# Optimization experiments

Measured on AMD Instinct MI355X. Metric: run time of the kernel, lower is better.

Reference implementation:

```python
import jax, jax.numpy as jnp
import numpy as np

N, B, DIN = 128, 2, 128
D, DFF, NHEAD, NLAYERS = 256, 1024, 8, 2
BLOCK = 32
LENGTH = 160


def setup_inputs() -> dict:
    key = jax.random.key(0)
    ks = jax.random.split(key, 10)
    r = lambda k, sh: jax.random.normal(k, sh, jnp.float32) * 0.05
    return {
        "inputs": jax.random.normal(ks[0], (N, B, DIN), jnp.float32),
        "in_W1": r(ks[1], (DIN, DFF)), "in_b1": jnp.zeros((DFF,), jnp.float32),
        "in_W2": r(ks[2], (DFF, D)), "in_b2": jnp.zeros((D,), jnp.float32),
        "k_W1": r(ks[3], (DIN, DFF)), "k_b1": jnp.zeros((DFF,), jnp.float32),
        "k_W2": r(ks[4], (DFF, 2)), "k_b2": jnp.zeros((2,), jnp.float32),
        "Wqkv": r(ks[5], (NLAYERS, D, 3 * D)), "bqkv": jnp.zeros((NLAYERS, 3 * D), jnp.float32),
        "Wo": r(ks[6], (NLAYERS, D, D)), "bo": jnp.zeros((NLAYERS, D), jnp.float32),
        "ln1_g": jnp.ones((NLAYERS, D), jnp.float32), "ln1_b": jnp.zeros((NLAYERS, D), jnp.float32),
        "W1": r(ks[7], (NLAYERS, D, DFF)), "b1": jnp.zeros((NLAYERS, DFF), jnp.float32),
        "W2": r(ks[8], (NLAYERS, DFF, D)), "b2": jnp.zeros((NLAYERS, D), jnp.float32),
        "ln2_g": jnp.ones((NLAYERS, D), jnp.float32), "ln2_b": jnp.zeros((NLAYERS, D), jnp.float32),
        "length": LENGTH,
    }


def _ln(x, g, b):
    m = jnp.mean(x, axis=-1, keepdims=True)
    v = jnp.mean(jnp.square(x - m), axis=-1, keepdims=True)
    return (x - m) * jax.lax.rsqrt(v + 1e-5) * g + b


def _forward(inputs, in_W1, in_b1, in_W2, in_b2, k_W1, k_b1, k_W2, k_b2,
             Wqkv, bqkv, Wo, bo, ln1_g, ln1_b, W1, b1, W2, b2, ln2_g, ln2_b, length):
    n, b, din = inputs.shape
    d = in_W2.shape[1]
    H, dh = NHEAD, in_W2.shape[1] // NHEAD
    Wmax = 2 * BLOCK + 1
    L = length
    idx = jnp.arange(n)
    starts = jnp.maximum(0, idx - BLOCK)                 # [N]
    ends = jnp.minimum(L, idx + BLOCK + 1)               # [N]
    cols = starts[:, None] + jnp.arange(Wmax)[None, :]   # [N,Wmax] absolute column per window slot
    valid = cols < ends[:, None]                          # [N,Wmax] ragged-window mask

    # sinusoidal PE at absolute column positions (start_idx = max(0, i-block))
    pos = cols.astype(jnp.float32)
    div = jnp.exp(jnp.arange(0, din, 2, dtype=jnp.float32) * (-np.log(10000.0) / din))
    ang = pos[..., None] * div                            # [N,Wmax,din/2]
    pe = jnp.stack([jnp.sin(ang), jnp.cos(ang)], axis=-1).reshape(n, Wmax, din)

    # row token repeated across its window + PE, then input_ff
    x = inputs[:, None, :, :] + pe[:, :, None, :]         # [N,Wmax,B,din]
    h = jnp.maximum(x @ in_W1 + in_b1, 0.0) @ in_W2 + in_b2  # [N,Wmax,B,D]

    # TransformerEncoder (post-norm, relu, eval mode) over the window axis, padded slots masked as keys
    kmask = valid[:, None, None, None, :]                 # [N,1,1,1,Wmax]
    scale = 1.0 / np.sqrt(dh)
    for l in range(Wqkv.shape[0]):
        qkv = h @ Wqkv[l] + bqkv[l]
        q, k, v = [t.reshape(n, Wmax, b, H, dh) for t in jnp.split(qkv, 3, axis=-1)]
        s = jnp.einsum('nqbhe,nkbhe->nbhqk', q, k) * scale
        s = jnp.where(kmask, s, -jnp.inf)
        a = jax.nn.softmax(s, axis=-1)
        o = jnp.einsum('nbhqk,nkbhe->nqbhe', a, v).reshape(n, Wmax, b, d)
        h = _ln(h + o @ Wo[l] + bo[l], ln1_g[l], ln1_b[l])
        f = jnp.maximum(h @ W1[l] + b1[l], 0.0) @ W2[l] + b2[l]
        h = _ln(h + f, ln2_g[l], ln2_b[l])

    # hierarchy kernel scores (Gaussian band kernel with learned (mu, logsig) per row/batch)
    kp = jnp.maximum(inputs @ k_W1 + k_b1, 0.0) @ k_W2 + k_b2   # [N,B,2]
    hscale = L / n
    diff = cols.astype(jnp.float32) - idx[:, None].astype(jnp.float32) * hscale  # [N,Wmax]
    hier = -jnp.square(diff[:, :, None] - kp[:, None, :, 0]) * jnp.exp(kp[:, None, :, 1])  # [N,Wmax,B]

    # scatter banded values/scores into dense [N,L,...] then row-softmax and weighted combine
    n_idx = jnp.broadcast_to(idx[:, None], (n, Wmax))
    scat = jnp.where(valid, cols, L)                      # out-of-bounds -> dropped
    v_mat = jnp.zeros((n, L, b, d), jnp.float32).at[n_idx, scat].set(h, mode='drop')
    h_mat = jnp.full((n, L, b), -jnp.inf, jnp.float32).at[n_idx, scat].set(hier, mode='drop')
    w = jax.nn.softmax(h_mat, axis=0)[..., None]          # softmax over rows per column
    return jnp.sum(v_mat * w, axis=0)                     # [L,B,D]


def reference(inputs, in_W1, in_b1, in_W2, in_b2, k_W1, k_b1, k_W2, k_b2,
              Wqkv, bqkv, Wo, bo, ln1_g, ln1_b, W1, b1, W2, b2, ln2_g, ln2_b, length):
    return _forward(inputs, in_W1, in_b1, in_W2, in_b2, k_W1, k_b1, k_W2, k_b2,
                    Wqkv, bqkv, Wo, bo, ln1_g, ln1_b, W1, b1, W2, b2, ln2_g, ln2_b, length)
```

## Files before the change

### kernel.cpp

```cpp
#include <hip/hip_runtime.h>

constexpr int NN    = 128;
constexpr int BB    = 2;
constexpr int DIN   = 128;
constexpr int DD    = 256;
constexpr int DFF   = 1024;
constexpr int NH    = 8;
constexpr int DH    = 32;
constexpr int NL    = 2;
constexpr int BLK   = 32;
constexpr int WMAX  = 2 * BLK + 1;
constexpr int RROWS = NN * WMAX * BB;

typedef __attribute__((ext_vector_type(8))) short s16x8;
typedef __attribute__((ext_vector_type(4))) float f32x4;

__device__ __forceinline__ ushort f2bf(float f) {
  unsigned u = __float_as_uint(f);
  unsigned r = (u + 0x7fffu + ((u >> 16) & 1u)) >> 16;
  return (ushort)r;
}
__device__ __forceinline__ float bf2f(ushort h) {
  return __uint_as_float(((unsigned)h) << 16);
}
__device__ __forceinline__ float bfl(unsigned u) { return __uint_as_float(u << 16); }
__device__ __forceinline__ float bfh(unsigned u) { return __uint_as_float(u & 0xffff0000u); }

__device__ __forceinline__ void gld16(const void* g, void* l) {
  __builtin_amdgcn_global_load_lds(
      (const __attribute__((address_space(1))) void*)g,
      (__attribute__((address_space(3))) void*)l, 16, 0, 0);
}
__device__ __forceinline__ void vmdrain() {
  asm volatile("s_waitcnt vmcnt(0)" ::: "memory");
}

struct TD { const float* in; ushort* out; int K; int N; };
struct TPack { TD d[10]; };
constexpr int WCONV_TILES = 1920;
constexpr int BX_BLOCKS   = RROWS * DIN / 256;

__global__ __launch_bounds__(256) void k_prep(
    TPack p, const float* __restrict__ inp, ushort* __restrict__ x,
    const float* __restrict__ kW1, const float* __restrict__ kb1,
    const float* __restrict__ kW2, const float* __restrict__ kb2,
    float* __restrict__ kp) {
  __shared__ float ls[32 * 33];
  int bid = blockIdx.x;
  int tid = threadIdx.x;
  if (bid < WCONV_TILES) {
    const int cum[11] = {0, 128, 384, 576, 768, 832, 896, 1152, 1408, 1664, 1920};
    int mi = 0;
#pragma unroll
    for (int i = 0; i < 10; ++i) if (bid >= cum[i + 1]) mi = i + 1;
    TD t = p.d[mi];
    int tile = bid - cum[mi];
    int ntk = t.K >> 5;
    int tn = tile / ntk, tk = tile - tn * ntk;
    int r = tid >> 5, c = tid & 31;
#pragma unroll
    for (int i = 0; i < 4; ++i) {
      int kk = r + 8 * i;
      ls[kk * 33 + c] = t.in[(size_t)(tk * 32 + kk) * t.N + tn * 32 + c];
    }
    __syncthreads();
#pragma unroll
    for (int i = 0; i < 4; ++i) {
      int rr = r + 8 * i;
      t.out[(size_t)(tn * 32 + rr) * t.K + tk * 32 + c] = f2bf(ls[c * 33 + rr]);
    }
  } else if (bid < WCONV_TILES + BX_BLOCKS) {
    int e = (bid - WCONV_TILES) * 256 + tid;
    int i = e & 127, r = e >> 7;
    int n = r / (WMAX * BB);
    int rem = r - n * (WMAX * BB);
    int w = rem >> 1, b = rem & 1;
    int st = n - BLK; if (st < 0) st = 0;
    float pos = (float)(st + w);
    float div = __expf(-0.0719557841f * (float)(i & 126));
    float ang = pos * div;
    float pe = (i & 1) ? __cosf(ang) : __sinf(ang);
    x[e] = f2bf(inp[(n * BB + b) * DIN + i] + pe);
  } else {
    int row = bid - (WCONV_TILES + BX_BLOCKS);
    float* xs = ls;
    float* red = ls + 256;
    if (tid < DIN) xs[tid] = inp[row * DIN + tid];
    __syncthreads();
    float a0 = 0.f, a1 = 0.f;
    for (int j = tid; j < DFF; j += 256) {
      float acc = kb1[j];
      for (int k = 0; k < DIN; ++k) acc += xs[k] * kW1[k * DFF + j];
      acc = fmaxf(acc, 0.f);
      a0 += acc * kW2[2 * j];
      a1 += acc * kW2[2 * j + 1];
    }
#pragma unroll
    for (int m = 32; m > 0; m >>= 1) {
      a0 += __shfl_xor(a0, m, 64);
      a1 += __shfl_xor(a1, m, 64);
    }
    if ((tid & 63) == 0) { red[(tid >> 6) * 2] = a0; red[(tid >> 6) * 2 + 1] = a1; }
    __syncthreads();
    if (tid == 0) {
      kp[row * 2 + 0] = red[0] + red[2] + red[4] + red[6] + kb2[0];
      kp[row * 2 + 1] = red[1] + red[3] + red[5] + red[7] + kb2[1];
    }
  }
}

template<int BMT, int RELU, int FUSE_LN, int DBUF>
__global__ __launch_bounds__(512) void k_gemm8(
    const ushort* __restrict__ A, const ushort* __restrict__ Bt,
    const float* __restrict__ bias, const ushort* __restrict__ resid,
    const float* __restrict__ lng, const float* __restrict__ lnb,
    ushort* __restrict__ out, int N, int K) {
  constexpr int MF = BMT / 32;
  constexpr int NB = DBUF ? 2 : 1;
  __shared__ __align__(16) char As[NB * BMT * 128];
  __shared__ __align__(16) char Bs[NB * 256 * 128];
  int tid = threadIdx.x;
  int m0 = blockIdx.x * BMT, n0 = blockIdx.y * 256;
  int lane = tid & 63, w = tid >> 6;
  int wr = w >> 2, wc = w & 3;
  int fr = lane & 15, g = lane >> 4;
  f32x4 acc[MF][4] = {};

  auto stage = [&](int half, int tk) {
    int kb = tk * 64;
    char* Ah = As + half * (BMT * 128);
    char* Bh = Bs + half * (256 * 128);
#pragma unroll
    for (int it = 0; it < BMT / 64; ++it) {
      int e = tid + it * 512;
      int row = e >> 3, c = e & 7;
      gld16(A + (size_t)(m0 + row) * K + kb + ((c ^ (row & 7)) * 8), Ah + e * 16);
    }
#pragma unroll
    for (int it = 0; it < 4; ++it) {
      int e = tid + it * 512;
      int row = e >> 3, c = e & 7;
      gld16(Bt + (size_t)(n0 + row) * K + kb + ((c ^ (row & 7)) * 8), Bh + e * 16);
    }
  };
  auto compute = [&](int half) {
    const char* Ah = As + half * (BMT * 128);
    const char* Bh = Bs + half * (256 * 128);
#pragma unroll
    for (int ks = 0; ks < 2; ++ks) {
      int kByte = ks * 64 + g * 16;
      s16x8 a[MF], b[4];
#pragma unroll
      for (int m = 0; m < MF; ++m) {
        int row = wr * (BMT / 2) + m * 16 + fr;
        a[m] = *(const s16x8*)(Ah + ((row * 128 + kByte) ^ ((row & 7) << 4)));
      }
#pragma unroll
      for (int n = 0; n < 4; ++n) {
        int row = wc * 64 + n * 16 + fr;
        b[n] = *(const s16x8*)(Bh + ((row * 128 + kByte) ^ ((row & 7) << 4)));
      }
#pragma unroll
      for (int m = 0; m < MF; ++m)
#pragma unroll
        for (int n = 0; n < 4; ++n)
          acc[m][n] = __builtin_amdgcn_mfma_f32_16x16x32_bf16(a[m], b[n], acc[m][n], 0, 0, 0);
    }
  };

  int nt = K >> 6;
  if constexpr (DBUF) {
    stage(0, 0);
    vmdrain();
    __syncthreads();
    for (int t = 0; t < nt; ++t) {
      if (t + 1 < nt) stage((t + 1) & 1, t + 1);
      compute(t & 1);
      vmdrain();
      __syncthreads();
    }
  } else {
    for (int t = 0; t < nt; ++t) {
      stage(0, t);
      vmdrain();
      __syncthreads();
      compute(0);
      __syncthreads();
    }
  }

  if constexpr (!FUSE_LN) {
#pragma unroll
    for (int m = 0; m < MF; ++m) {
      int rowb = m0 + wr * (BMT / 2) + m * 16 + g * 4;
#pragma unroll
      for (int n = 0; n < 4; ++n) {
        int col = n0 + wc * 64 + n * 16 + fr;
        float bv = bias[col];
#pragma unroll
        for (int j = 0; j < 4; ++j) {
          float v = acc[m][n][j] + bv;
          if (RELU) v = fmaxf(v, 0.f);
          out[(size_t)(rowb + j) * N + col] = f2bf(v);
        }
      }
    }
  } else {
    float* psum = (float*)As;
    float* psq  = (float*)(As + 4 * BMT * 4);
#pragma unroll
    for (int m = 0; m < MF; ++m) {
      int rowb = wr * (BMT / 2) + m * 16 + g * 4;
#pragma unroll
      for (int j = 0; j < 4; ++j) {
        float ps = 0.f, pq = 0.f;
#pragma unroll
        for (int n = 0; n < 4; ++n) {
          int col = wc * 64 + n * 16 + fr;
          float v = acc[m][n][j] + bias[col]
                  + bf2f(resid[(size_t)(m0 + rowb + j) * 256 + col]);
          acc[m][n][j] = v;
          ps += v; pq += v * v;
        }
#pragma unroll
        for (int d = 1; d < 16; d <<= 1) {
          ps += __shfl_xor(ps, d, 64);
          pq += __shfl_xor(pq, d, 64);
        }
        if (fr == 0) { psum[wc * BMT + rowb + j] = ps; psq[wc * BMT + rowb + j] = pq; }
      }
    }
    __syncthreads();
#pragma unroll
    for (int m = 0; m < MF; ++m) {
      int rowb = wr * (BMT / 2) + m * 16 + g * 4;
#pragma unroll
      for (int j = 0; j < 4; ++j) {
        int lr = rowb + j;
        float sm = psum[lr] + psum[BMT + lr] + psum[2 * BMT + lr] + psum[3 * BMT + lr];
        float sq = psq[lr] + psq[BMT + lr] + psq[2 * BMT + lr] + psq[3 * BMT + lr];
        float mean = sm * (1.f / 256.f);
        float var = sq * (1.f / 256.f) - mean * mean;
        float rs = rsqrtf(var + 1e-5f);
#pragma unroll
        for (int n = 0; n < 4; ++n) {
          int col = wc * 64 + n * 16 + fr;
          float v = (acc[m][n][j] - mean) * rs * lng[col] + lnb[col];
          out[(size_t)(m0 + lr) * 256 + col] = f2bf(v);
        }
      }
    }
  }
}

constexpr int QKS = 40;
constexpr int VTS = 104;
constexpr int PS  = 104;

__device__ __forceinline__ int vslot(int d, int r) {
  int rc = r >> 3;
  int sw = (rc < 8) ? (rc ^ (d >> 3)) : rc;
  return d * VTS + sw * 8 + (r & 7);
}

__global__ __launch_bounds__(320) void k_attn(
    const ushort* __restrict__ qkv, ushort* __restrict__ o,
    const int* __restrict__ lenp) {
  __shared__ __align__(16) ushort Ks[80 * QKS];
  __shared__ __align__(16) ushort Vt[32 * VTS];
  __shared__ __align__(16) ushort Pb[5 * 16 * PS];
  int L = lenp[0];
  int blk = blockIdx.x;
  int hh = blk & 7;
  int nb = blk >> 3;
  int b = nb & 1;
  int n = nb >> 1;
  int s0 = n - BLK; if (s0 < 0) s0 = 0;
  int e0 = n + BLK + 1; if (e0 > L) e0 = L;
  int vn = e0 - s0;
  int tid = threadIdx.x;

  for (int i = tid; i < 32 * VTS / 2; i += 320) ((uint*)Vt)[i] = 0;
  for (int i = tid; i < 15 * QKS / 2; i += 320)
    ((uint*)(Ks + 65 * QKS))[i] = 0;
  __syncthreads();
  for (int e = tid; e < 65 * 4; e += 320) {
    int r = e >> 2, c = e & 3;
    const ushort* base = qkv + ((size_t)(n * WMAX + r) * BB + b) * (3 * DD) + hh * DH;
    *(uint4*)(Ks + r * QKS + c * 8) = *(const uint4*)(base + DD + c * 8);
    uint4 vv = *(const uint4*)(base + 2 * DD + c * 8);
    const ushort* vp = (const ushort*)&vv;
#pragma unroll
    for (int u = 0; u < 8; ++u) Vt[vslot(c * 8 + u, r)] = vp[u];
  }

  int w = tid >> 6, lane = tid & 63;
  int fr = lane & 15, g = lane >> 4;
  int q0 = w * 16;
  ushort* Pw = Pb + w * 16 * PS;

  int qr_ld = q0 + fr; if (qr_ld > 64) qr_ld = 64;
  s16x8 aq = *(const s16x8*)(qkv + ((size_t)(n * WMAX + qr_ld) * BB + b) * (3 * DD)
                             + hh * DH + g * 8);
  __syncthreads();

  f32x4 sacc[5];
#pragma unroll
  for (int t = 0; t < 5; ++t) {
    s16x8 bk = *(const s16x8*)(Ks + (t * 16 + fr) * QKS + g * 8);
    f32x4 z = {0.f, 0.f, 0.f, 0.f};
    sacc[t] = __builtin_amdgcn_mfma_f32_16x16x32_bf16(aq, bk, z, 0, 0, 0);
  }
  const float scl = 0.17677669529663687f;
#pragma unroll
  for (int j = 0; j < 4; ++j) {
    float pv[5];
    float mx = -3e38f;
#pragma unroll
    for (int t = 0; t < 5; ++t) {
      bool ok = (t * 16 + fr) < vn;
      pv[t] = ok ? sacc[t][j] * scl : -3e38f;
      mx = fmaxf(mx, pv[t]);
    }
#pragma unroll
    for (int d = 1; d < 16; d <<= 1) mx = fmaxf(mx, __shfl_xor(mx, d, 64));
    float sum = 0.f;
#pragma unroll
    for (int t = 0; t < 5; ++t) {
      float e = ((t * 16 + fr) < vn) ? __expf(pv[t] - mx) : 0.f;
      pv[t] = e;
      sum += e;
    }
#pragma unroll
    for (int d = 1; d < 16; d <<= 1) sum += __shfl_xor(sum, d, 64);
    float inv = 1.f / sum;
#pragma unroll
    for (int t = 0; t < 5; ++t)
      Pw[(g * 4 + j) * PS + t * 16 + fr] = f2bf(pv[t] * inv);
  }
  {
    int zr = lane >> 2, zc = 80 + (lane & 3) * 4;
    *(uint2*)(Pw + zr * PS + zc) = make_uint2(0u, 0u);
  }
  __syncthreads();

  f32x4 oacc[2] = {};
#pragma unroll
  for (int k0 = 0; k0 < 3; ++k0) {
    s16x8 ap = *(const s16x8*)(Pw + fr * PS + k0 * 32 + g * 8);
#pragma unroll
    for (int nt = 0; nt < 2; ++nt) {
      s16x8 bv = *(const s16x8*)(Vt + vslot(nt * 16 + fr, k0 * 32 + g * 8));
      oacc[nt] = __builtin_amdgcn_mfma_f32_16x16x32_bf16(ap, bv, oacc[nt], 0, 0, 0);
    }
  }
#pragma unroll
  for (int nt = 0; nt < 2; ++nt) {
#pragma unroll
    for (int j = 0; j < 4; ++j) {
      int qr = q0 + g * 4 + j;
      if (qr < WMAX)
        o[((size_t)(n * WMAX + qr) * BB + b) * DD + hh * DH + nt * 16 + fr] =
            f2bf(oacc[nt][j]);
    }
  }
}

__global__ __launch_bounds__(256) void k_final(
    const ushort* __restrict__ h, const float* __restrict__ kp,
    float* __restrict__ out, const int* __restrict__ lenp) {
  int L = lenp[0];
  int t = blockIdx.x >> 1, b = blockIdx.x & 1;
  float hsc = (float)L / (float)NN;
  int nlo = t - BLK; if (nlo < 0) nlo = 0;
  int nhi = t + BLK; if (nhi > NN - 1) nhi = NN - 1;
  float mx = -3e38f;
  for (int n = nlo; n <= nhi; ++n) {
    float kp0 = kp[(n * BB + b) * 2 + 0];
    float kp1 = kp[(n * BB + b) * 2 + 1];
    float dif = (float)t - (float)n * hsc - kp0;
    float lg = -dif * dif * __expf(kp1);
    mx = fmaxf(mx, lg);
  }
  float sum = 0.f, acc = 0.f;
  int c = threadIdx.x;
  for (int n = nlo; n <= nhi; ++n) {
    float kp0 = kp[(n * BB + b) * 2 + 0];
    float kp1 = kp[(n * BB + b) * 2 + 1];
    float dif = (float)t - (float)n * hsc - kp0;
    float lg = -dif * dif * __expf(kp1);
    float p = __expf(lg - mx);
    sum += p;
    int st = n - BLK; if (st < 0) st = 0;
    int w = t - st;
    acc += p * bf2f(h[(size_t)((n * WMAX + w) * BB + b) * DD + c]);
  }
  out[(size_t)(t * BB + b) * DD + c] = acc / sum;
}

extern "C" void kernel_launch(void* const* d_in, const int* in_sizes, int n_in,
                              void* d_out, int out_size, void* d_ws, size_t ws_size,
                              hipStream_t stream) {
  const float* inputs = (const float*)d_in[0];
  const float* in_W1  = (const float*)d_in[1];
  const float* in_b1  = (const float*)d_in[2];
  const float* in_W2  = (const float*)d_in[3];
  const float* in_b2  = (const float*)d_in[4];
  const float* k_W1   = (const float*)d_in[5];
  const float* k_b1   = (const float*)d_in[6];
  const float* k_W2   = (const float*)d_in[7];
  const float* k_b2   = (const float*)d_in[8];
  const float* Wqkv   = (const float*)d_in[9];
  const float* bqkv   = (const float*)d_in[10];
  const float* Wo     = (const float*)d_in[11];
  const float* bo     = (const float*)d_in[12];
  const float* ln1_g  = (const float*)d_in[13];
  const float* ln1_b  = (const float*)d_in[14];
  const float* W1     = (const float*)d_in[15];
  const float* b1     = (const float*)d_in[16];
  const float* W2     = (const float*)d_in[17];
  const float* b2     = (const float*)d_in[18];
  const float* ln2_g  = (const float*)d_in[19];
  const float* ln2_b  = (const float*)d_in[20];
  const int*   lenp   = (const int*)d_in[21];
  float* out = (float*)d_out;
  (void)in_sizes; (void)n_in; (void)ws_size;

  ushort* wsu = (ushort*)d_ws;
  size_t off = 0;
  auto alloc = [&](size_t nelem) { ushort* p = wsu + off; off += (nelem + 7) & ~7ull; return p; };
  ushort* inW1t = alloc((size_t)DFF * DIN);
  ushort* inW2t = alloc((size_t)DD * DFF);
  ushort* Wqkvt = alloc((size_t)NL * 3 * DD * DD);
  ushort* Wot   = alloc((size_t)NL * DD * DD);
  ushort* W1t   = alloc((size_t)NL * DFF * DD);
  ushort* W2t   = alloc((size_t)NL * DD * DFF);
  ushort* x     = alloc((size_t)RROWS * DIN);
  ushort* tq    = alloc((size_t)RROWS * DFF);
  ushort* hb    = alloc((size_t)RROWS * DD);
  ushort* ob    = alloc((size_t)RROWS * DD);
  float*  kp    = (float*)(wsu + off);

  int L = out_size / (BB * DD);

  TPack tp;
  tp.d[0] = {in_W1, inW1t, DIN, DFF};
  tp.d[1] = {in_W2, inW2t, DFF, DD};
  tp.d[2] = {Wqkv,                        Wqkvt,                       DD, 3 * DD};
  tp.d[3] = {Wqkv + (size_t)DD * 3 * DD,  Wqkvt + (size_t)3 * DD * DD, DD, 3 * DD};
  tp.d[4] = {Wo,                    Wot,                   DD, DD};
  tp.d[5] = {Wo + (size_t)DD * DD,  Wot + (size_t)DD * DD, DD, DD};
  tp.d[6] = {W1,                      W1t,                    DD, DFF};
  tp.d[7] = {W1 + (size_t)DD * DFF,   W1t + (size_t)DFF * DD, DD, DFF};
  tp.d[8] = {W2,                      W2t,                    DFF, DD};
  tp.d[9] = {W2 + (size_t)DFF * DD,   W2t + (size_t)DD * DFF, DFF, DD};

  k_prep<<<WCONV_TILES + BX_BLOCKS + NN * BB, 256, 0, stream>>>(
      tp, inputs, x, k_W1, k_b1, k_W2, k_b2, kp);

  k_gemm8<128, 1, 0, 0><<<dim3(RROWS / 128, 4), 512, 0, stream>>>(
      x, inW1t, in_b1, nullptr, nullptr, nullptr, tq, DFF, DIN);
  k_gemm8<64, 0, 0, 1><<<dim3(RROWS / 64, 1), 512, 0, stream>>>(
      tq, inW2t, in_b2, nullptr, nullptr, nullptr, hb, DD, DFF);

  for (int l = 0; l < NL; ++l) {
    k_gemm8<128, 0, 0, 0><<<dim3(RROWS / 128, 3), 512, 0, stream>>>(
        hb, Wqkvt + (size_t)l * 3 * DD * DD, bqkv + (size_t)l * 3 * DD,
        nullptr, nullptr, nullptr, tq, 3 * DD, DD);
    k_attn<<<NN * BB * NH, 320, 0, stream>>>(tq, ob, lenp);
    k_gemm8<64, 0, 1, 1><<<dim3(RROWS / 64, 1), 512, 0, stream>>>(
        ob, Wot + (size_t)l * DD * DD, bo + (size_t)l * DD, hb,
        ln1_g + (size_t)l * DD, ln1_b + (size_t)l * DD, hb, DD, DD);
    k_gemm8<128, 1, 0, 0><<<dim3(RROWS / 128, 4), 512, 0, stream>>>(
        hb, W1t + (size_t)l * DFF * DD, b1 + (size_t)l * DFF,
        nullptr, nullptr, nullptr, tq, DFF, DD);
    k_gemm8<64, 0, 1, 1><<<dim3(RROWS / 64, 1), 512, 0, stream>>>(
        tq, W2t + (size_t)l * DD * DFF, b2 + (size_t)l * DD, hb,
        ln2_g + (size_t)l * DD, ln2_b + (size_t)l * DD, hb, DD, DFF);
  }
  k_final<<<L * BB, 256, 0, stream>>>(hb, kp, out, lenp);
}
```

Baseline: 268.1 us.

## Fuse input MLP and post-attention layer GEMMs into single kernels

Replaces the two-GEMM input MLP with one kernel that computes the DFF hidden activation in 64-column chunks kept in LDS and immediately multiplies by W2. It also fuses the output projection, first LayerNorm, FFN up, ReLU, FFN down and second LayerNorm into one per-row-tile kernel. This is meant to avoid writing and re-reading the large DFF intermediate through global memory and to cut kernel launches. In exchange it uses large LDS (about 108 KB per block), which limits occupancy, and the chunked loop has many barriers and little overlap between weight loads and compute.

```diff
diff --git a/kernel.cpp b/kernel.cpp
--- a/kernel.cpp
+++ b/kernel.cpp
@@ -23,8 +23,6 @@
 __device__ __forceinline__ float bf2f(ushort h) {
   return __uint_as_float(((unsigned)h) << 16);
 }
-__device__ __forceinline__ float bfl(unsigned u) { return __uint_as_float(u << 16); }
-__device__ __forceinline__ float bfh(unsigned u) { return __uint_as_float(u & 0xffff0000u); }
 
 __device__ __forceinline__ void gld16(const void* g, void* l) {
   __builtin_amdgcn_global_load_lds(
@@ -109,16 +107,13 @@
   }
 }
 
-template<int BMT, int RELU, int FUSE_LN, int DBUF>
+template<int BMT>
 __global__ __launch_bounds__(512) void k_gemm8(
     const ushort* __restrict__ A, const ushort* __restrict__ Bt,
-    const float* __restrict__ bias, const ushort* __restrict__ resid,
-    const float* __restrict__ lng, const float* __restrict__ lnb,
-    ushort* __restrict__ out, int N, int K) {
+    const float* __restrict__ bias, ushort* __restrict__ out, int N, int K) {
   constexpr int MF = BMT / 32;
-  constexpr int NB = DBUF ? 2 : 1;
-  __shared__ __align__(16) char As[NB * BMT * 128];
-  __shared__ __align__(16) char Bs[NB * 256 * 128];
+  __shared__ __align__(16) char As[BMT * 128];
+  __shared__ __align__(16) char Bs[256 * 128];
   int tid = threadIdx.x;
   int m0 = blockIdx.x * BMT, n0 = blockIdx.y * 256;
   int lane = tid & 63, w = tid >> 6;
@@ -126,26 +121,22 @@
   int fr = lane & 15, g = lane >> 4;
   f32x4 acc[MF][4] = {};
 
-  auto stage = [&](int half, int tk) {
-    int kb = tk * 64;
-    char* Ah = As + half * (BMT * 128);
-    char* Bh = Bs + half * (256 * 128);
+  for (int kb = 0; kb < K; kb += 64) {
+    __syncthreads();
 #pragma unroll
     for (int it = 0; it < BMT / 64; ++it) {
       int e = tid + it * 512;
       int row = e >> 3, c = e & 7;
-      gld16(A + (size_t)(m0 + row) * K + kb + ((c ^ (row & 7)) * 8), Ah + e * 16);
+      gld16(A + (size_t)(m0 + row) * K + kb + ((c ^ (row & 7)) * 8), As + e * 16);
     }
 #pragma unroll
     for (int it = 0; it < 4; ++it) {
       int e = tid + it * 512;
       int row = e >> 3, c = e & 7;
-      gld16(Bt + (size_t)(n0 + row) * K + kb + ((c ^ (row & 7)) * 8), Bh + e * 16);
-    }
-  };
-  auto compute = [&](int half) {
-    const char* Ah = As + half * (BMT * 128);
-    const char* Bh = Bs + half * (256 * 128);
+      gld16(Bt + (size_t)(n0 + row) * K + kb + ((c ^ (row & 7)) * 8), Bs + e * 16);
+    }
+    vmdrain();
+    __syncthreads();
 #pragma unroll
     for (int ks = 0; ks < 2; ++ks) {
       int kByte = ks * 64 + g * 16;
@@ -153,12 +144,12 @@
 #pragma unroll
       for (int m = 0; m < MF; ++m) {
         int row = wr * (BMT / 2) + m * 16 + fr;
-        a[m] = *(const s16x8*)(Ah + ((row * 128 + kByte) ^ ((row & 7) << 4)));
+        a[m] = *(const s16x8*)(As + ((row * 128 + kByte) ^ ((row & 7) << 4)));
       }
 #pragma unroll
       for (int n = 0; n < 4; ++n) {
         int row = wc * 64 + n * 16 + fr;
-        b[n] = *(const s16x8*)(Bh + ((row * 128 + kByte) ^ ((row & 7) << 4)));
+        b[n] = *(const s16x8*)(Bs + ((row * 128 + kByte) ^ ((row & 7) << 4)));
       }
 #pragma unroll
       for (int m = 0; m < MF; ++m)
@@ -166,88 +157,367 @@
         for (int n = 0; n < 4; ++n)
           acc[m][n] = __builtin_amdgcn_mfma_f32_16x16x32_bf16(a[m], b[n], acc[m][n], 0, 0, 0);
     }
+  }
+#pragma unroll
+  for (int m = 0; m < MF; ++m) {
+    int rowb = m0 + wr * (BMT / 2) + m * 16 + g * 4;
+#pragma unroll
+    for (int n = 0; n < 4; ++n) {
+      int col = n0 + wc * 64 + n * 16 + fr;
+      float bv = bias[col];
+#pragma unroll
+      for (int j = 0; j < 4; ++j)
+        out[(size_t)(rowb + j) * N + col] = f2bf(acc[m][n][j] + bv);
+    }
+  }
+}
+
+__global__ __launch_bounds__(512) void k_inmlp(
+    const ushort* __restrict__ x, const ushort* __restrict__ W1t,
+    const float* __restrict__ b1, const ushort* __restrict__ W2t,
+    const float* __restrict__ b2, ushort* __restrict__ hb) {
+  __shared__ __align__(16) char lds[73728];
+  char* xs  = lds;
+  char* ts  = lds + 16384;
+  char* w1b = lds + 24576;
+  char* w2b = lds + 40960;
+  int tid = threadIdx.x;
+  int m0 = blockIdx.x * 64;
+  int lane = tid & 63, w = tid >> 6;
+  int wr = w >> 2, wc = w & 3;
+  int fr = lane & 15, g = lane >> 4;
+
+  auto stW1 = [&](int c) {
+    int e = tid;
+#pragma unroll
+    for (int it = 0; it < 2; ++it, e += 512) {
+      int kt = e >> 9, row = (e >> 3) & 63, c8 = e & 7;
+      gld16(W1t + (size_t)(c * 64 + row) * 128 + kt * 64 + ((c8 ^ (row & 7)) * 8),
+            w1b + e * 16);
+    }
   };
-
-  int nt = K >> 6;
-  if constexpr (DBUF) {
-    stage(0, 0);
+  auto stW2 = [&](int c) {
+    int e = tid;
+#pragma unroll
+    for (int it = 0; it < 4; ++it, e += 512) {
+      int row = e >> 3, c8 = e & 7;
+      gld16(W2t + (size_t)row * 1024 + c * 64 + ((c8 ^ (row & 7)) * 8), w2b + e * 16);
+    }
+  };
+  {
+    int e = tid;
+#pragma unroll
+    for (int it = 0; it < 2; ++it, e += 512) {
+      int kt = e >> 9, row = (e >> 3) & 63, c8 = e & 7;
+      gld16(x + (size_t)(m0 + row) * 128 + kt * 64 + ((c8 ^ (row & 7)) * 8), xs + e * 16);
+    }
+  }
+  stW1(0);
+  vmdrain();
+  __syncthreads();
+
+  f32x4 acc2[2][4] = {};
+  for (int c = 0; c < 16; ++c) {
+    stW2(c);
+    f32x4 t1[2] = {};
+#pragma unroll
+    for (int kt = 0; kt < 2; ++kt)
+#pragma unroll
+      for (int ks = 0; ks < 2; ++ks) {
+        int kByte = ks * 64 + g * 16;
+        int brow = wc * 16 + fr;
+        s16x8 bfrag = *(const s16x8*)(w1b + kt * 8192 +
+                        ((brow * 128 + kByte) ^ ((brow & 7) << 4)));
+#pragma unroll
+        for (int m = 0; m < 2; ++m) {
+          int row = wr * 32 + m * 16 + fr;
+          s16x8 afrag = *(const s16x8*)(xs + kt * 8192 +
+                          ((row * 128 + kByte) ^ ((row & 7) << 4)));
+          t1[m] = __builtin_amdgcn_mfma_f32_16x16x32_bf16(afrag, bfrag, t1[m], 0, 0, 0);
+        }
+      }
     vmdrain();
     __syncthreads();
-    for (int t = 0; t < nt; ++t) {
-      if (t + 1 < nt) stage((t + 1) & 1, t + 1);
-      compute(t & 1);
-      vmdrain();
-      __syncthreads();
-    }
-  } else {
-    for (int t = 0; t < nt; ++t) {
-      stage(0, t);
-      vmdrain();
-      __syncthreads();
-      compute(0);
-      __syncthreads();
-    }
-  }
-
-  if constexpr (!FUSE_LN) {
-#pragma unroll
-    for (int m = 0; m < MF; ++m) {
-      int rowb = m0 + wr * (BMT / 2) + m * 16 + g * 4;
+    {
+      int col = wc * 16 + fr;
+      float bv = b1[c * 64 + col];
+#pragma unroll
+      for (int m = 0; m < 2; ++m) {
+        int rowb = wr * 32 + m * 16 + g * 4;
+#pragma unroll
+        for (int j = 0; j < 4; ++j) {
+          int r = rowb + j;
+          *(ushort*)(ts + ((r * 128 + col * 2) ^ ((r & 7) << 4))) =
+              f2bf(fmaxf(t1[m][j] + bv, 0.f));
+        }
+      }
+    }
+    if (c < 15) stW1(c + 1);
+    __syncthreads();
+#pragma unroll
+    for (int ks = 0; ks < 2; ++ks) {
+      int kByte = ks * 64 + g * 16;
+      s16x8 afrag[2];
+#pragma unroll
+      for (int m = 0; m < 2; ++m) {
+        int row = wr * 32 + m * 16 + fr;
+        afrag[m] = *(const s16x8*)(ts + ((row * 128 + kByte) ^ ((row & 7) << 4)));
+      }
 #pragma unroll
       for (int n = 0; n < 4; ++n) {
-        int col = n0 + wc * 64 + n * 16 + fr;
-        float bv = bias[col];
+        int row = wc * 64 + n * 16 + fr;
+        s16x8 bfrag = *(const s16x8*)(w2b + ((row * 128 + kByte) ^ ((row & 7) << 4)));
+#pragma unroll
+        for (int m = 0; m < 2; ++m)
+          acc2[m][n] = __builtin_amdgcn_mfma_f32_16x16x32_bf16(afrag[m], bfrag, acc2[m][n], 0, 0, 0);
+      }
+    }
+    vmdrain();
+    __syncthreads();
+  }
+#pragma unroll
+  for (int m = 0; m < 2; ++m) {
+    int rowb = m0 + wr * 32 + m * 16 + g * 4;
+#pragma unroll
+    for (int n = 0; n < 4; ++n) {
+      int col = wc * 64 + n * 16 + fr;
+      float bv = b2[col];
+#pragma unroll
+      for (int j = 0; j < 4; ++j)
+        hb[(size_t)(rowb + j) * 256 + col] = f2bf(acc2[m][n][j] + bv);
+    }
+  }
+}
+
+__global__ __launch_bounds__(512) void k_layer(
+    const ushort* __restrict__ ob, const ushort* __restrict__ Wot,
+    const float* __restrict__ bo, const float* __restrict__ ln1g,
+    const float* __restrict__ ln1b, const ushort* __restrict__ W1t,
+    const float* __restrict__ b1, const ushort* __restrict__ W2t,
+    const float* __restrict__ b2, const float* __restrict__ ln2g,
+    const float* __restrict__ ln2b, ushort* __restrict__ hb) {
+  __shared__ __align__(16) char lds[108544];
+  char* h1s = lds;
+  char* ts  = lds + 32768;
+  char* w1b = lds + 40960;
+  char* w2b = lds + 73728;
+  float* psum = (float*)(lds + 106496);
+  float* psq  = (float*)(lds + 106496 + 1024);
+  int tid = threadIdx.x;
+  int m0 = blockIdx.x * 64;
+  int lane = tid & 63, w = tid >> 6;
+  int wr = w >> 2, wc = w & 3;
+  int fr = lane & 15, g = lane >> 4;
+
+  auto stOA = [&](int half, int t) {
+    int e = tid;
+    int row = e >> 3, c8 = e & 7;
+    gld16(ob + (size_t)(m0 + row) * 256 + t * 64 + ((c8 ^ (row & 7)) * 8),
+          h1s + half * 8192 + e * 16);
+  };
+  auto stOB = [&](char* buf, int t) {
+    int e = tid;
+#pragma unroll
+    for (int it = 0; it < 4; ++it, e += 512) {
+      int row = e >> 3, c8 = e & 7;
+      gld16(Wot + (size_t)row * 256 + t * 64 + ((c8 ^ (row & 7)) * 8), buf + e * 16);
+    }
+  };
+  f32x4 acc1[2][4] = {};
+  stOA(0, 0); stOB(w1b, 0);
+  vmdrain();
+  __syncthreads();
+  for (int t = 0; t < 4; ++t) {
+    if (t < 3) { stOA((t + 1) & 1, t + 1); stOB((t & 1) ? w1b : w2b, t + 1); }
+    const char* Ah = h1s + (t & 1) * 8192;
+    const char* Bh = (t & 1) ? w2b : w1b;
+#pragma unroll
+    for (int ks = 0; ks < 2; ++ks) {
+      int kByte = ks * 64 + g * 16;
+      s16x8 a[2];
+#pragma unroll
+      for (int m = 0; m < 2; ++m) {
+        int row = wr * 32 + m * 16 + fr;
+        a[m] = *(const s16x8*)(Ah + ((row * 128 + kByte) ^ ((row & 7) << 4)));
+      }
+#pragma unroll
+      for (int n = 0; n < 4; ++n) {
+        int row = wc * 64 + n * 16 + fr;
+        s16x8 b = *(const s16x8*)(Bh + ((row * 128 + kByte) ^ ((row & 7) << 4)));
+#pragma unroll
+        for (int m = 0; m < 2; ++m)
+          acc1[m][n] = __builtin_amdgcn_mfma_f32_16x16x32_bf16(a[m], b, acc1[m][n], 0, 0, 0);
+      }
+    }
+    vmdrain();
+    __syncthreads();
+  }
+
+  auto stW1 = [&](int c) {
+    int e = tid;
+#pragma unroll
+    for (int it = 0; it < 4; ++it, e += 512) {
+      int kt = e >> 9, row = (e >> 3) & 63, c8 = e & 7;
+      gld16(W1t + (size_t)(c * 64 + row) * 256 + kt * 64 + ((c8 ^ (row & 7)) * 8),
+            w1b + e * 16);
+    }
+  };
+  auto stW2 = [&](int c) {
+    int e = tid;
+#pragma unroll
+    for (int it = 0; it < 4; ++it, e += 512) {
+      int row = e >> 3, c8 = e & 7;
+      gld16(W2t + (size_t)row * 1024 + c * 64 + ((c8 ^ (row & 7)) * 8), w2b + e * 16);
+    }
+  };
+  stW1(0);
+
+#pragma unroll
+  for (int m = 0; m < 2; ++m) {
+    int rowb = wr * 32 + m * 16 + g * 4;
+#pragma unroll
+    for (int j = 0; j < 4; ++j) {
+      int r = rowb + j;
+      float ps = 0.f, pq = 0.f;
+#pragma unroll
+      for (int n = 0; n < 4; ++n) {
+        int col = wc * 64 + n * 16 + fr;
+        float v = acc1[m][n][j] + bo[col] + bf2f(hb[(size_t)(m0 + r) * 256 + col]);
+        acc1[m][n][j] = v;
+        ps += v; pq += v * v;
+      }
+#pragma unroll
+      for (int d = 1; d < 16; d <<= 1) {
+        ps += __shfl_xor(ps, d, 64);
+        pq += __shfl_xor(pq, d, 64);
+      }
+      if (fr == 0) { psum[wc * 64 + r] = ps; psq[wc * 64 + r] = pq; }
+    }
+  }
+  __syncthreads();
+#pragma unroll
+  for (int m = 0; m < 2; ++m) {
+    int rowb = wr * 32 + m * 16 + g * 4;
+#pragma unroll
+    for (int j = 0; j < 4; ++j) {
+      int r = rowb + j;
+      float sm = psum[r] + psum[64 + r] + psum[128 + r] + psum[192 + r];
+      float sq = psq[r] + psq[64 + r] + psq[128 + r] + psq[192 + r];
+      float mean = sm * (1.f / 256.f);
+      float var = sq * (1.f / 256.f) - mean * mean;
+      float rs = rsqrtf(var + 1e-5f);
+#pragma unroll
+      for (int n = 0; n < 4; ++n) {
+        int col = wc * 64 + n * 16 + fr;
+        float v = (acc1[m][n][j] - mean) * rs * ln1g[col] + ln1b[col];
+        *(ushort*)(h1s + wc * 8192 + ((r * 128 + (col & 63) * 2) ^ ((r & 7) << 4))) = f2bf(v);
+      }
+    }
+  }
+  vmdrain();
+  __syncthreads();
+
+  f32x4 acc2[2][4] = {};
+  for (int c = 0; c < 16; ++c) {
+    stW2(c);
+    f32x4 t1[2] = {};
+#pragma unroll
+    for (int kt = 0; kt < 4; ++kt)
+#pragma unroll
+      for (int ks = 0; ks < 2; ++ks) {
+        int kByte = ks * 64 + g * 16;
+        int brow = wc * 16 + fr;
+        s16x8 bfrag = *(const s16x8*)(w1b + kt * 8192 +
+                        ((brow * 128 + kByte) ^ ((brow & 7) << 4)));
+#pragma unroll
+        for (int m = 0; m < 2; ++m) {
+          int row = wr * 32 + m * 16 + fr;
+          s16x8 afrag = *(const s16x8*)(h1s + kt * 8192 +
+                          ((row * 128 + kByte) ^ ((row & 7) << 4)));
+          t1[m] = __builtin_amdgcn_mfma_f32_16x16x32_bf16(afrag, bfrag, t1[m], 0, 0, 0);
+        }
+      }
+    vmdrain();
+    __syncthreads();
+    {
+      int col = wc * 16 + fr;
+      float bv = b1[c * 64 + col];
+#pragma unroll
+      for (int m = 0; m < 2; ++m) {
+        int rowb = wr * 32 + m * 16 + g * 4;
 #pragma unroll
         for (int j = 0; j < 4; ++j) {
-          float v = acc[m][n][j] + bv;
-          if (RELU) v = fmaxf(v, 0.f);
-          out[(size_t)(rowb + j) * N + col] = f2bf(v);
+          int r = rowb + j;
+          *(ushort*)(ts + ((r * 128 + col * 2) ^ ((r & 7) << 4))) =
+              f2bf(fmaxf(t1[m][j] + bv, 0.f));
         }
       }
     }
-  } else {
-    float* psum = (float*)As;
-    float* psq  = (float*)(As + 4 * BMT * 4);
-#pragma unroll
-    for (int m = 0; m < MF; ++m) {
-      int rowb = wr * (BMT / 2) + m * 16 + g * 4;
-#pragma unroll
-      for (int j = 0; j < 4; ++j) {
-        float ps = 0.f, pq = 0.f;
-#pragma unroll
-        for (int n = 0; n < 4; ++n) {
-          int col = wc * 64 + n * 16 + fr;
-          float v = acc[m][n][j] + bias[col]
-                  + bf2f(resid[(size_t)(m0 + rowb + j) * 256 + col]);
-          acc[m][n][j] = v;
-          ps += v; pq += v * v;
-        }
-#pragma unroll
-        for (int d = 1; d < 16; d <<= 1) {
-          ps += __shfl_xor(ps, d, 64);
-          pq += __shfl_xor(pq, d, 64);
-        }
-        if (fr == 0) { psum[wc * BMT + rowb + j] = ps; psq[wc * BMT + rowb + j] = pq; }
-      }
-    }
-    __syncthreads();
-#pragma unroll
-    for (int m = 0; m < MF; ++m) {
-      int rowb = wr * (BMT / 2) + m * 16 + g * 4;
-#pragma unroll
-      for (int j = 0; j < 4; ++j) {
-        int lr = rowb + j;
-        float sm = psum[lr] + psum[BMT + lr] + psum[2 * BMT + lr] + psum[3 * BMT + lr];
-        float sq = psq[lr] + psq[BMT + lr] + psq[2 * BMT + lr] + psq[3 * BMT + lr];
-        float mean = sm * (1.f / 256.f);
-        float var = sq * (1.f / 256.f) - mean * mean;
-        float rs = rsqrtf(var + 1e-5f);
-#pragma unroll
-        for (int n = 0; n < 4; ++n) {
-          int col = wc * 64 + n * 16 + fr;
-          float v = (acc[m][n][j] - mean) * rs * lng[col] + lnb[col];
-          out[(size_t)(m0 + lr) * 256 + col] = f2bf(v);
-        }
+    if (c < 15) stW1(c + 1);
+    __syncthreads();
+#pragma unroll
+    for (int ks = 0; ks < 2; ++ks) {
+      int kByte = ks * 64 + g * 16;
+      s16x8 afrag[2];
+#pragma unroll
+      for (int m = 0; m < 2; ++m) {
+        int row = wr * 32 + m * 16 + fr;
+        afrag[m] = *(const s16x8*)(ts + ((row * 128 + kByte) ^ ((row & 7) << 4)));
+      }
+#pragma unroll
+      for (int n = 0; n < 4; ++n) {
+        int row = wc * 64 + n * 16 + fr;
+        s16x8 bfrag = *(const s16x8*)(w2b + ((row * 128 + kByte) ^ ((row & 7) << 4)));
+#pragma unroll
+        for (int m = 0; m < 2; ++m)
+          acc2[m][n] = __builtin_amdgcn_mfma_f32_16x16x32_bf16(afrag[m], bfrag, acc2[m][n], 0, 0, 0);
+      }
+    }
+    vmdrain();
+    __syncthreads();
+  }
+
+#pragma unroll
+  for (int m = 0; m < 2; ++m) {
+    int rowb = wr * 32 + m * 16 + g * 4;
+#pragma unroll
+    for (int j = 0; j < 4; ++j) {
+      int r = rowb + j;
+      float ps = 0.f, pq = 0.f;
+#pragma unroll
+      for (int n = 0; n < 4; ++n) {
+        int col = wc * 64 + n * 16 + fr;
+        float h1v = bf2f(*(const ushort*)(h1s + wc * 8192 +
+                       ((r * 128 + (col & 63) * 2) ^ ((r & 7) << 4))));
+        float v = acc2[m][n][j] + b2[col] + h1v;
+        acc2[m][n][j] = v;
+        ps += v; pq += v * v;
+      }
+#pragma unroll
+      for (int d = 1; d < 16; d <<= 1) {
+        ps += __shfl_xor(ps, d, 64);
+        pq += __shfl_xor(pq, d, 64);
+      }
+      if (fr == 0) { psum[wc * 64 + r] = ps; psq[wc * 64 + r] = pq; }
+    }
+  }
+  __syncthreads();
+#pragma unroll
+  for (int m = 0; m < 2; ++m) {
+    int rowb = wr * 32 + m * 16 + g * 4;
+#pragma unroll
+    for (int j = 0; j < 4; ++j) {
+      int r = rowb + j;
+      float sm = psum[r] + psum[64 + r] + psum[128 + r] + psum[192 + r];
+      float sq = psq[r] + psq[64 + r] + psq[128 + r] + psq[192 + r];
+      float mean = sm * (1.f / 256.f);
+      float var = sq * (1.f / 256.f) - mean * mean;
+      float rs = rsqrtf(var + 1e-5f);
+#pragma unroll
+      for (int n = 0; n < 4; ++n) {
+        int col = wc * 64 + n * 16 + fr;
+        float v = (acc2[m][n][j] - mean) * rs * ln2g[col] + ln2b[col];
+        hb[(size_t)(m0 + r) * 256 + col] = f2bf(v);
       }
     }
   }
@@ -436,7 +706,7 @@
   ushort* W1t   = alloc((size_t)NL * DFF * DD);
   ushort* W2t   = alloc((size_t)NL * DD * DFF);
   ushort* x     = alloc((size_t)RROWS * DIN);
-  ushort* tq    = alloc((size_t)RROWS * DFF);
+  ushort* tq    = alloc((size_t)RROWS * 3 * DD);
   ushort* hb    = alloc((size_t)RROWS * DD);
   ushort* ob    = alloc((size_t)RROWS * DD);
   float*  kp    = (float*)(wsu + off);
@@ -458,25 +728,19 @@
   k_prep<<<WCONV_TILES + BX_BLOCKS + NN * BB, 256, 0, stream>>>(
       tp, inputs, x, k_W1, k_b1, k_W2, k_b2, kp);
 
-  k_gemm8<128, 1, 0, 0><<<dim3(RROWS / 128, 4), 512, 0, stream>>>(
-      x, inW1t, in_b1, nullptr, nullptr, nullptr, tq, DFF, DIN);
-  k_gemm8<64, 0, 0, 1><<<dim3(RROWS / 64, 1), 512, 0, stream>>>(
-      tq, inW2t, in_b2, nullptr, nullptr, nullptr, hb, DD, DFF);
+  k_inmlp<<<RROWS / 64, 512, 0, stream>>>(x, inW1t, in_b1, inW2t, in_b2, hb);
 
   for (int l = 0; l < NL; ++l) {
-    k_gemm8<128, 0, 0, 0><<<dim3(RROWS / 128, 3), 512, 0, stream>>>(
+    k_gemm8<128><<<dim3(RROWS / 128, 3), 512, 0, stream>>>(
         hb, Wqkvt + (size_t)l * 3 * DD * DD, bqkv + (size_t)l * 3 * DD,
-        nullptr, nullptr, nullptr, tq, 3 * DD, DD);
+        tq, 3 * DD, DD);
     k_attn<<<NN * BB * NH, 320, 0, stream>>>(tq, ob, lenp);
-    k_gemm8<64, 0, 1, 1><<<dim3(RROWS / 64, 1), 512, 0, stream>>>(
-        ob, Wot + (size_t)l * DD * DD, bo + (size_t)l * DD, hb,
-        ln1_g + (size_t)l * DD, ln1_b + (size_t)l * DD, hb, DD, DD);
-    k_gemm8<128, 1, 0, 0><<<dim3(RROWS / 128, 4), 512, 0, stream>>>(
-        hb, W1t + (size_t)l * DFF * DD, b1 + (size_t)l * DFF,
-        nullptr, nullptr, nullptr, tq, DFF, DD);
-    k_gemm8<64, 0, 1, 1><<<dim3(RROWS / 64, 1), 512, 0, stream>>>(
-        tq, W2t + (size_t)l * DD * DFF, b2 + (size_t)l * DD, hb,
-        ln2_g + (size_t)l * DD, ln2_b + (size_t)l * DD, hb, DD, DFF);
+    k_layer<<<RROWS / 64, 512, 0, stream>>>(
+        ob, Wot + (size_t)l * DD * DD, bo + (size_t)l * DD,
+        ln1_g + (size_t)l * DD, ln1_b + (size_t)l * DD,
+        W1t + (size_t)l * DFF * DD, b1 + (size_t)l * DFF,
+        W2t + (size_t)l * DD * DFF, b2 + (size_t)l * DD,
+        ln2_g + (size_t)l * DD, ln2_b + (size_t)l * DD, hb);
   }
   k_final<<<L * BB, 256, 0, stream>>>(hb, kp, out, lenp);
 }
```

Result: slower. 294.9 us (+10.0%).
